# Kernel tuning notes

Measured on AMD Instinct MI355X. Metric: run time of the kernel, lower is better.

## Reference

```python
import jax, jax.numpy as jnp
from jax import lax
import numpy as np

CONF_THRESH = 0.015
NMS_DIST = 4
BORDER = 4
RED = 8


def setup_inputs() -> dict:
    key = jax.random.key(0)
    k1, k2, k3, k4, k5 = jax.random.split(key, 5)
    B, C, H, W = 32, 128, 64, 64
    MID, NCLS = 256, RED * RED + 1
    return {
        "x": jax.random.normal(k1, (B, C, H, W), dtype=jnp.float32),
        "w1": jax.random.normal(k2, (MID, C, 3, 3), dtype=jnp.float32) * 0.05,
        "b1": jax.random.normal(k3, (MID,), dtype=jnp.float32) * 0.05,
        "w2": jax.random.normal(k4, (NCLS, MID, 1, 1), dtype=jnp.float32) * 0.05,
        "b2": jax.random.normal(k5, (NCLS,), dtype=jnp.float32) * 0.05,
    }


def _conv3x3(x, w, b):
    y = lax.conv_general_dilated(
        x, w, window_strides=(1, 1), padding="SAME",
        dimension_numbers=("NCHW", "OIHW", "NCHW"))
    return y + b[None, :, None, None]


def _max_pool(s, r):
    # s: [B, H, W]; infinity-norm neighborhood max, window (2r+1)x(2r+1)
    return lax.reduce_window(
        s, -jnp.inf, lax.max,
        window_dimensions=(1, 2 * r + 1, 2 * r + 1),
        window_strides=(1, 1, 1), padding="SAME")


def _grid_nms(scores, r, iters=8):
    # Iterated local-max suppression; converges to the greedy (sorted-by-score)
    # grid NMS of the original nms_fast routine for distinct scores.
    zeros = jnp.zeros_like(scores)
    max_mask = (scores == _max_pool(scores, r)) & (scores > 0)
    for _ in range(iters):
        supp = _max_pool(max_mask.astype(scores.dtype), r) > 0
        supp_scores = jnp.where(supp, zeros, scores)
        new_max = (supp_scores == _max_pool(supp_scores, r)) & (supp_scores > 0)
        max_mask = max_mask | (new_max & ~supp)
    return jnp.where(max_mask, scores, zeros)


def reference(x, w1, b1, w2, b2):
    B, _, hh, ww = x.shape
    h = jax.nn.relu(_conv3x3(x, w1, b1))                       # [B, mid, hh, ww]
    semi = jnp.einsum("bchw,oc->bohw", h, w2[:, :, 0, 0]) + b2[None, :, None, None]
    dense = jax.nn.softmax(semi, axis=1)                        # [B, 65, hh, ww]
    nodust = dense[:, :-1]                                      # drop dust bin
    # depth-to-space: [B,64,hh,ww] -> [B, hh*8, ww*8]
    heat = nodust.transpose(0, 2, 3, 1).reshape(B, hh, ww, RED, RED)
    heat = heat.transpose(0, 1, 3, 2, 4).reshape(B, hh * RED, ww * RED)
    # confidence threshold
    scores = jnp.where(heat >= CONF_THRESH, heat, 0.0)
    # grid-based NMS (dense keep-map formulation of nms_fast)
    kept = _grid_nms(scores, NMS_DIST)
    # border removal
    Hi, Wi = hh * RED, ww * RED
    yy = jnp.arange(Hi)
    xx = jnp.arange(Wi)
    border = ((yy[:, None] >= BORDER) & (yy[:, None] < Hi - BORDER) &
              (xx[None, :] >= BORDER) & (xx[None, :] < Wi - BORDER))
    return kept * border[None, :, :].astype(kept.dtype)
```

## Files before the change

### kernel.cpp

```cpp
#include <hip/hip_runtime.h>
#include <hip/hip_bf16.h>
#include <stdint.h>

#define BATCH 32
#define CIN 128
#define HH 64
#define WW 64
#define MID 256
#define NCLS 65
#define HI 512
#define NWORDS 8
#define HBS2 264
#define SEMS 68
#define RMS 68

typedef _Float16 half8 __attribute__((ext_vector_type(8)));
typedef _Float16 half4v __attribute__((ext_vector_type(4)));
typedef _Float16 half2v __attribute__((ext_vector_type(2)));
typedef float f32x4 __attribute__((ext_vector_type(4)));

__global__ __launch_bounds__(256) void prep_wf(
    const float* __restrict__ w1, const float* __restrict__ w2,
    _Float16* __restrict__ w1fh, _Float16* __restrict__ w1fl,
    _Float16* __restrict__ w2fh, _Float16* __restrict__ w2fl,
    int* __restrict__ flags)
{
    if (blockIdx.x == 0 && threadIdx.x < 16) flags[threadIdx.x] = 0;
    const int idx = blockIdx.x * 256 + threadIdx.x;
    if (idx < 294912) {
        const int j = idx & 7, lane = (idx >> 3) & 63, mt = (idx >> 9) & 15;
        const int s = (idx >> 13) & 3, kix = idx >> 15;
        const int m = mt * 16 + (lane & 15);
        const int c = s * 32 + (lane >> 4) * 8 + j;
        const int ky = kix / 3, kx = kix - ky * 3;
        const float v = w1[((m * CIN + c) * 3 + ky) * 3 + kx];
        const _Float16 hi = (_Float16)v;
        w1fh[idx] = hi;
        w1fl[idx] = (_Float16)(v - (float)hi);
    } else {
        const int i2 = idx - 294912;
        const int j = i2 & 7, lane = (i2 >> 3) & 63;
        const int ks = (i2 >> 9) & 7, mt = i2 >> 12;
        const int o = mt * 16 + (lane & 15);
        const int k = ks * 32 + (lane >> 4) * 8 + j;
        const float v = (o < NCLS) ? w2[o * MID + k] : 0.f;
        const _Float16 hi = (_Float16)v;
        w2fh[i2] = hi;
        w2fl[i2] = (_Float16)(v - (float)hi);
    }
}

__global__ __launch_bounds__(256, 3) void head_kernel(
    const float* __restrict__ x,
    const _Float16* __restrict__ w1fh, const _Float16* __restrict__ w1fl,
    const _Float16* __restrict__ w2fh, const _Float16* __restrict__ w2fl,
    const float* __restrict__ b1, const float* __restrict__ b2,
    float* __restrict__ out)
{
    const int b  = blockIdx.z;
    const int y0 = blockIdx.y * 8, x0 = blockIdx.x * 8;
    const int tid = threadIdx.x;
    const int lane = tid & 63, w = tid >> 6;
    const int n = lane & 15, q = lane >> 4;

    __shared__ __align__(16) unsigned char SM[51200];
    char* const xhb = (char*)SM;
    _Float16* const hbh = (_Float16*)SM;
    _Float16* const hbl = hbh + 32 * HBS2;
    float* const sem  = (float*)(SM + 33792);
    float* const rinv = sem + 32 * SEMS;

    const float* xb = x + (size_t)b * CIN * HH * WW;
    for (int i = tid; i < 6400; i += 256) {
        const int c2 = i / 100, pos = i - c2 * 100;
        const int r = pos / 10, cc = pos - r * 10;
        const int gy = y0 - 1 + r, gx = x0 - 1 + cc;
        float v0 = 0.f, v1 = 0.f;
        if ((unsigned)gy < HH && (unsigned)gx < WW) {
            const float* p = xb + (c2 * 2 * HH + gy) * WW + gx;
            v0 = p[0]; v1 = p[HH * WW];
        }
        const _Float16 h0 = (_Float16)v0, h1 = (_Float16)v1;
        half2v hi = {h0, h1};
        half2v lo = {(_Float16)(v0 - (float)h0), (_Float16)(v1 - (float)h1)};
        const int slot = (c2 >> 2) ^ (pos & 15);
        char* p16 = xhb + pos * 256 + (slot << 4) + (c2 & 3) * 4;
        *(half2v*)p16 = hi;
        *(half2v*)(p16 + 25600) = lo;
    }
    __syncthreads();

    f32x4 acc[4][4];
#pragma unroll
    for (int i = 0; i < 4; ++i)
#pragma unroll
        for (int t = 0; t < 4; ++t) acc[i][t] = (f32x4){0.f, 0.f, 0.f, 0.f};

    int bposT[4];
#pragma unroll
    for (int t = 0; t < 4; ++t)
        bposT[t] = (t * 2 + (n >> 3)) * 10 + (n & 7);

    for (int kix = 0; kix < 9; ++kix) {
        const int ky = kix / 3;
        const int koff = ky * 10 + (kix - ky * 3);
#pragma unroll
        for (int s = 0; s < 4; ++s) {
            half8 Bh[4], Bl[4];
#pragma unroll
            for (int t = 0; t < 4; ++t) {
                const int pos = bposT[t] + koff;
                const int byteoff = pos * 256 +
                    ((((s << 2) + q) ^ (pos & 15)) << 4);
                Bh[t] = *(const half8*)(xhb + byteoff);
                Bl[t] = *(const half8*)(xhb + 25600 + byteoff);
            }
#pragma unroll
            for (int i = 0; i < 4; ++i) {
                const size_t o = (size_t)(kix * 4 + s) * 8192 +
                                 (w * 4 + i) * 512 + lane * 8;
                const half8 Ah = *(const half8*)(w1fh + o);
                const half8 Al = *(const half8*)(w1fl + o);
#pragma unroll
                for (int t = 0; t < 4; ++t) {
                    acc[i][t] = __builtin_amdgcn_mfma_f32_16x16x32_f16(
                        Ah, Bh[t], acc[i][t], 0, 0, 0);
                    acc[i][t] = __builtin_amdgcn_mfma_f32_16x16x32_f16(
                        Ah, Bl[t], acc[i][t], 0, 0, 0);
                    acc[i][t] = __builtin_amdgcn_mfma_f32_16x16x32_f16(
                        Al, Bh[t], acc[i][t], 0, 0, 0);
                }
            }
        }
    }
    __syncthreads();

    for (int hf = 0; hf < 2; ++hf) {
        if (hf) __syncthreads();
#pragma unroll
        for (int i = 0; i < 4; ++i)
#pragma unroll
            for (int tt = 0; tt < 2; ++tt) {
                const int t = hf * 2 + tt;
                const int p = tt * 16 + n;
                const int m0 = w * 64 + i * 16 + q * 4;
                const f32x4 a = acc[i][t];
                const float4 bv = *(const float4*)(b1 + m0);
                const float h0 = fmaxf(a[0] + bv.x, 0.f);
                const float h1 = fmaxf(a[1] + bv.y, 0.f);
                const float h2 = fmaxf(a[2] + bv.z, 0.f);
                const float h3 = fmaxf(a[3] + bv.w, 0.f);
                half4v hh = {(_Float16)h0, (_Float16)h1,
                             (_Float16)h2, (_Float16)h3};
                half4v hl = {(_Float16)(h0 - (float)hh[0]),
                             (_Float16)(h1 - (float)hh[1]),
                             (_Float16)(h2 - (float)hh[2]),
                             (_Float16)(h3 - (float)hh[3])};
                *(half4v*)(hbh + p * HBS2 + m0) = hh;
                *(half4v*)(hbl + p * HBS2 + m0) = hl;
            }
        __syncthreads();
        {
            const int nt = w & 1;
            const int mt0 = (w < 2) ? 0 : 3;
            const int nmt = (w < 2) ? 3 : 2;
            const int pb = nt * 16 + n;
            f32x4 a2[3];
#pragma unroll
            for (int j = 0; j < 3; ++j) a2[j] = (f32x4){0.f, 0.f, 0.f, 0.f};
#pragma unroll
            for (int ks = 0; ks < 8; ++ks) {
                const int ad = pb * HBS2 + ks * 32 + q * 8;
                const half8 B2h = *(const half8*)(hbh + ad);
                const half8 B2l = *(const half8*)(hbl + ad);
#pragma unroll
                for (int j = 0; j < 3; ++j)
                    if (j < nmt) {
                        const size_t o = (size_t)((mt0 + j) * 8 + ks) * 512 +
                                         lane * 8;
                        const half8 A2h = *(const half8*)(w2fh + o);
                        const half8 A2l = *(const half8*)(w2fl + o);
                        a2[j] = __builtin_amdgcn_mfma_f32_16x16x32_f16(
                            A2h, B2h, a2[j], 0, 0, 0);
                        a2[j] = __builtin_amdgcn_mfma_f32_16x16x32_f16(
                            A2h, B2l, a2[j], 0, 0, 0);
                        a2[j] = __builtin_amdgcn_mfma_f32_16x16x32_f16(
                            A2l, B2h, a2[j], 0, 0, 0);
                    }
            }
#pragma unroll
            for (int j = 0; j < 3; ++j)
                if (j < nmt) {
                    const int o0 = (mt0 + j) * 16 + q * 4;
#pragma unroll
                    for (int r2 = 0; r2 < 4; ++r2) {
                        const int o = o0 + r2;
                        if (o < NCLS)
                            sem[pb * SEMS + o] = a2[j][r2] + b2[o];
                    }
                }
        }
        __syncthreads();
        if (tid < 128) {
            const int p = tid >> 2, q4 = tid & 3;
            const int o0 = q4 * 17;
            const int o1 = (o0 + 17 < NCLS) ? o0 + 17 : NCLS;
            float mx = -1e30f;
            for (int o = o0; o < o1; ++o)
                mx = fmaxf(mx, sem[p * SEMS + o]);
            mx = fmaxf(mx, __shfl_xor(mx, 1));
            mx = fmaxf(mx, __shfl_xor(mx, 2));
            float ssum = 0.f;
            for (int o = o0; o < o1; ++o) {
                float e = __expf(sem[p * SEMS + o] - mx);
                sem[p * SEMS + o] = e;
                ssum += e;
            }
            ssum += __shfl_xor(ssum, 1);
            ssum += __shfl_xor(ssum, 2);
            if (q4 == 0) rinv[p] = 1.f / ssum;
        }
        __syncthreads();
        for (int t2 = tid; t2 < 2048; t2 += 256) {
            const int p = t2 >> 6, o = t2 & 63;
            float v = sem[p * SEMS + o] * rinv[p];
            if (!(v >= 0.015f)) v = 0.f;
            const int P = hf * 32 + p;
            const int py = P >> 3, px = P & 7;
            const int row = (y0 + py) * 8 + (o >> 3);
            const int col = (x0 + px) * 8 + (o & 7);
            out[((size_t)b * HI + row) * HI + col] = v;
        }
    }
}

__device__ __forceinline__ void nms_hmax_phase(
    const float* __restrict__ Sb, const uint64_t* __restrict__ sup,
    float* __restrict__ rm, int ty, int tx, int tid, int rbase)
{
    const int lane = tid & 63;
    for (int k = tid; k < 640; k += 256) {
        const int rr = k >> 4, g = k & 15;
        const int r = rbase + rr;
        const int gy = ty - 4 + r;
        const int x4 = g * 4;
        const uint64_t* sr = sup + r * 3;
        float own[4] = {0.f, 0.f, 0.f, 0.f};
        float halo[4] = {0.f, 0.f, 0.f, 0.f};
        if ((unsigned)gy < HI) {
            const float* row = Sb + (size_t)gy * HI;
            const float4 o4 = *(const float4*)(row + tx + x4);
            own[0] = o4.x; own[1] = o4.y; own[2] = o4.z; own[3] = o4.w;
            const uint64_t w1 = sr[1];
#pragma unroll
            for (int cc = 0; cc < 4; ++cc)
                if ((w1 >> (x4 + cc)) & 1ull) own[cc] = 0.f;
            if (g == 0 && tx >= 4) {
                const float4 h4 = *(const float4*)(row + tx - 4);
                halo[0] = h4.x; halo[1] = h4.y; halo[2] = h4.z; halo[3] = h4.w;
                const uint64_t w0 = sr[0];
#pragma unroll
                for (int cc = 0; cc < 4; ++cc)
                    if ((w0 >> (60 + cc)) & 1ull) halo[cc] = 0.f;
            } else if (g == 15 && tx + 64 < HI) {
                const float4 h4 = *(const float4*)(row + tx + 64);
                halo[0] = h4.x; halo[1] = h4.y; halo[2] = h4.z; halo[3] = h4.w;
                const uint64_t w2 = sr[2];
#pragma unroll
                for (int cc = 0; cc < 4; ++cc)
                    if ((w2 >> cc) & 1ull) halo[cc] = 0.f;
            }
        }
        float v[12];
#pragma unroll
        for (int cc = 0; cc < 4; ++cc) {
            v[4 + cc] = own[cc];
            v[cc]     = __shfl(own[cc], lane - 1);
            v[8 + cc] = __shfl(own[cc], lane + 1);
        }
        if (g == 0) {
#pragma unroll
            for (int cc = 0; cc < 4; ++cc) v[cc] = halo[cc];
        } else if (g == 15) {
#pragma unroll
            for (int cc = 0; cc < 4; ++cc) v[8 + cc] = halo[cc];
        }
        const float m4567 = fmaxf(fmaxf(v[4],v[5]), fmaxf(v[6],v[7]));
        const float m23 = fmaxf(v[2],v[3]), m89 = fmaxf(v[8],v[9]);
        const float o0 = fmaxf(fmaxf(fmaxf(v[0],v[1]), m23),
                               fmaxf(m4567, v[8]));
        const float o1 = fmaxf(fmaxf(v[1], m23), fmaxf(m4567, m89));
        const float o2 = fmaxf(fmaxf(m23, m4567), fmaxf(m89, v[10]));
        const float o3 = fmaxf(fmaxf(v[3], m4567),
                               fmaxf(fmaxf(m89, v[10]), v[11]));
        *(float4*)(rm + rr * RMS + x4) = make_float4(o0,o1,o2,o3);
    }
}

__global__ __launch_bounds__(256, 8) void nms_iter(
    const float* __restrict__ S, const uint64_t* __restrict__ Min,
    uint64_t* __restrict__ Mout, int* __restrict__ flags, int chk, int set)
{
    const int b = blockIdx.z;
    const int bx = blockIdx.x;
    const int ty = blockIdx.y * 64, tx = bx * 64;
    const int tid = threadIdx.x;

    if (chk >= 0 && flags[chk] == 0) {
        for (int y = tid; y < 64; y += 256)
            Mout[((size_t)b * HI + ty + y) * NWORDS + bx] =
                Min[((size_t)b * HI + ty + y) * NWORDS + bx];
        return;
    }

    __shared__ uint64_t smw[80 * 3];
    __shared__ uint64_t hd[80 * 3];
    __shared__ uint64_t sup[72 * 3];
    __shared__ __align__(16) float rm[40 * RMS];

    const float* Sb = S + (size_t)b * HI * HI;
    int chg = 0;

    if (Min) {
        if (tid < 240) {
            const int i = tid / 3, j = tid % 3;
            const int yy = ty - 8 + i;
            const int wj = bx - 1 + j;
            uint64_t v = 0;
            if ((unsigned)yy < HI && (unsigned)wj < NWORDS)
                v = Min[((size_t)b * HI + yy) * NWORDS + wj];
            smw[tid] = v;
        }
        __syncthreads();
        if (tid < 240) {
            const int j = tid % 3;
            const uint64_t c = smw[tid];
            const uint64_t l = j > 0 ? smw[tid - 1] : 0ull;
            const uint64_t r = j < 2 ? smw[tid + 1] : 0ull;
            uint64_t d = c;
#pragma unroll
            for (int s = 1; s <= 4; ++s)
                d |= (c >> s) | (r << (64 - s)) | (c << s) | (l >> (64 - s));
            hd[tid] = d;
        }
        __syncthreads();
        if (tid < 216) {
            uint64_t v = 0;
#pragma unroll
            for (int k = 0; k < 9; ++k) v |= hd[tid + 3 * k];
            sup[tid] = v;
        }
        __syncthreads();
    } else {
        if (tid < 240) smw[tid] = 0;
        if (tid < 216) sup[tid] = 0;
        __syncthreads();
    }

    for (int half = 0; half < 2; ++half) {
        const int rbase = half * 32;
        nms_hmax_phase(Sb, sup, rm, ty, tx, tid, rbase);
        __syncthreads();
        {
            const int wv = tid >> 6, lane = tid & 63;
            const int rb = wv * 8;
            const int ybase = rbase + rb;
            float ring[9];
#pragma unroll
            for (int k = 0; k < 8; ++k) ring[k] = rm[(rb + k) * RMS + lane];
#pragma unroll
            for (int qq = 0; qq < 8; ++qq) {
                const int y = ybase + qq;
                ring[(qq + 8) % 9] = rm[(rb + qq + 8) * RMS + lane];
                float mv = ring[0];
#pragma unroll
                for (int k = 1; k < 9; ++k) mv = fmaxf(mv, ring[k]);
                float c = Sb[(size_t)(ty + y) * HI + tx + lane];
                if ((sup[(y + 4) * 3 + 1] >> lane) & 1ull) c = 0.f;
                const uint64_t oldw = smw[(y + 8) * 3 + 1];
                const bool keep = ((oldw >> lane) & 1ull) ||
                                  (c > 0.f && c == mv);
                const uint64_t word = __ballot(keep);
                if (lane == 0) {
                    Mout[((size_t)b * HI + ty + y) * NWORDS + bx] = word;
                    if (word != oldw) chg = 1;
                }
            }
        }
        __syncthreads();
    }
    if (set >= 0 && (tid & 63) == 0 && chg) flags[set] = 1;
}

__global__ __launch_bounds__(256, 8) void nms_last(
    const float* __restrict__ S, const uint64_t* __restrict__ Min,
    float* __restrict__ out, const int* __restrict__ flags)
{
    const int b = blockIdx.z;
    const int bx = blockIdx.x;
    const int ty = blockIdx.y * 64, tx = bx * 64;
    const int tid = threadIdx.x;

    const float* Sb = S + (size_t)b * HI * HI;

    if (flags[7] == 0) {
        for (int k = tid; k < 1024; k += 256) {
            const int r = k >> 4, c4 = k & 15;
            const int gy = ty + r;
            const int gx0 = tx + c4 * 4;
            const uint64_t w = Min[((size_t)b * HI + gy) * NWORDS + bx];
            float4 v = *(const float4*)(Sb + (size_t)gy * HI + gx0);
            float* pv = (float*)&v;
            const bool rowok = (gy >= 4) && (gy < HI - 4);
#pragma unroll
            for (int cc = 0; cc < 4; ++cc) {
                const int xx = gx0 + cc;
                const bool keep = rowok && (xx >= 4) && (xx < HI - 4) &&
                                  ((w >> ((c4 * 4 + cc) & 63)) & 1ull);
                if (!keep) pv[cc] = 0.f;
            }
            *(float4*)(out + ((size_t)b * HI + gy) * HI + gx0) = v;
        }
        return;
    }

    __shared__ uint64_t smw[80 * 3];
    __shared__ uint64_t hd[80 * 3];
    __shared__ uint64_t sup[72 * 3];
    __shared__ __align__(16) float rm[40 * RMS];

    if (tid < 240) {
        const int i = tid / 3, j = tid % 3;
        const int yy = ty - 8 + i;
        const int wj = bx - 1 + j;
        uint64_t v = 0;
        if ((unsigned)yy < HI && (unsigned)wj < NWORDS)
            v = Min[((size_t)b * HI + yy) * NWORDS + wj];
        smw[tid] = v;
    }
    __syncthreads();
    if (tid < 240) {
        const int j = tid % 3;
        const uint64_t c = smw[tid];
        const uint64_t l = j > 0 ? smw[tid - 1] : 0ull;
        const uint64_t r = j < 2 ? smw[tid + 1] : 0ull;
        uint64_t d = c;
#pragma unroll
        for (int s = 1; s <= 4; ++s)
            d |= (c >> s) | (r << (64 - s)) | (c << s) | (l >> (64 - s));
        hd[tid] = d;
    }
    __syncthreads();
    if (tid < 216) {
        uint64_t v = 0;
#pragma unroll
        for (int k = 0; k < 9; ++k) v |= hd[tid + 3 * k];
        sup[tid] = v;
    }
    __syncthreads();

    for (int half = 0; half < 2; ++half) {
        const int rbase = half * 32;
        nms_hmax_phase(Sb, sup, rm, ty, tx, tid, rbase);
        __syncthreads();
        {
            const int wv = tid >> 6, lane = tid & 63;
            const int rb = wv * 8;
            const int ybase = rbase + rb;
            float ring[9];
#pragma unroll
            for (int k = 0; k < 8; ++k) ring[k] = rm[(rb + k) * RMS + lane];
#pragma unroll
            for (int qq = 0; qq < 8; ++qq) {
                const int y = ybase + qq;
                ring[(qq + 8) % 9] = rm[(rb + qq + 8) * RMS + lane];
                float mv = ring[0];
#pragma unroll
                for (int k = 1; k < 9; ++k) mv = fmaxf(mv, ring[k]);
                const int gy = ty + y, gx = tx + lane;
                const float corig = Sb[(size_t)gy * HI + gx];
                float c = corig;
                if ((sup[(y + 4) * 3 + 1] >> lane) & 1ull) c = 0.f;
                const uint64_t oldw = smw[(y + 8) * 3 + 1];
                const bool keep = ((oldw >> lane) & 1ull) ||
                                  (c > 0.f && c == mv);
                const bool border = (gy >= 4) && (gy < HI - 4) &&
                                    (gx >= 4) && (gx < HI - 4);
                out[((size_t)b * HI + gy) * HI + gx] =
                    (keep && border) ? corig : 0.f;
            }
        }
        __syncthreads();
    }
}

__global__ __launch_bounds__(256) void finalize_bits(
    float* __restrict__ S, const uint64_t* __restrict__ Mw)
{
    const int i4 = blockIdx.x * 256 + threadIdx.x;
    const size_t base = (size_t)i4 * 4;
    const int x = (int)(base & 511);
    const int y = (int)((base >> 9) & 511);
    const int bb = (int)(base >> 18);
    const uint64_t w = Mw[((size_t)bb * HI + y) * NWORDS + (x >> 6)];
    float4 v = ((const float4*)S)[i4];
    float* pv = (float*)&v;
    const bool rowok = (y >= 4) && (y < HI - 4);
#pragma unroll
    for (int cc = 0; cc < 4; ++cc) {
        const int xx = x + cc;
        const bool keep = rowok && (xx >= 4) && (xx < HI - 4) &&
                          ((w >> (xx & 63)) & 1ull);
        if (!keep) pv[cc] = 0.f;
    }
    ((float4*)S)[i4] = v;
}

extern "C" void kernel_launch(void* const* d_in, const int* in_sizes, int n_in,
                              void* d_out, int out_size, void* d_ws, size_t ws_size,
                              hipStream_t stream) {
    const float* x  = (const float*)d_in[0];
    const float* w1 = (const float*)d_in[1];
    const float* b1 = (const float*)d_in[2];
    const float* w2 = (const float*)d_in[3];
    const float* b2 = (const float*)d_in[4];
    float* out = (float*)d_out;

    char* wsb = (char*)d_ws;
    _Float16* w1fh = (_Float16*)(wsb);
    _Float16* w1fl = (_Float16*)(wsb + 0x90000);
    _Float16* w2fh = (_Float16*)(wsb + 0x120000);
    _Float16* w2fl = (_Float16*)(wsb + 0x130000);
    int* flags     = (int*)(wsb + 0x13B000);
    uint64_t* MA   = (uint64_t*)(wsb + 0x140000);
    uint64_t* MB   = (uint64_t*)(wsb + 0x240000);

    const size_t S_OFF = 0x340000;
    const size_t S_BYTES = (size_t)BATCH * HI * HI * 4;
    const bool use_ws = ws_size >= S_OFF + S_BYTES;
    float* S = use_ws ? (float*)(wsb + S_OFF) : out;

    prep_wf<<<1232, 256, 0, stream>>>(w1, w2, w1fh, w1fl, w2fh, w2fl, flags);
    head_kernel<<<dim3(8, 8, BATCH), 256, 0, stream>>>(
        x, w1fh, w1fl, w2fh, w2fl, b1, b2, S);

    dim3 g(NWORDS, 8, BATCH);
    nms_iter<<<g, 256, 0, stream>>>(S, nullptr, MA, flags, -1, -1);
    nms_iter<<<g, 256, 0, stream>>>(S, MA, MB, flags, -1, 1);
    nms_iter<<<g, 256, 0, stream>>>(S, MB, MA, flags, 1, 2);
    nms_iter<<<g, 256, 0, stream>>>(S, MA, MB, flags, 2, 3);
    nms_iter<<<g, 256, 0, stream>>>(S, MB, MA, flags, 3, 4);
    nms_iter<<<g, 256, 0, stream>>>(S, MA, MB, flags, 4, 5);
    nms_iter<<<g, 256, 0, stream>>>(S, MB, MA, flags, 5, 6);
    nms_iter<<<g, 256, 0, stream>>>(S, MA, MB, flags, 6, 7);

    if (use_ws) {
        nms_last<<<g, 256, 0, stream>>>(S, MB, out, flags);
    } else {
        nms_iter<<<g, 256, 0, stream>>>(S, MB, MA, flags, 7, -1);
        const int nf4 = BATCH * HI * HI / 4;
        finalize_bits<<<nf4 / 256, 256, 0, stream>>>(out, MA);
    }
}
```

Baseline: 495.4 us.

## Halve head kernel shared memory by staging input channels in two halves

The head kernel now loads the input tile in two channel halves, running the conv K-loop over each half, so its shared buffer shrinks from 51200 to 25600 bytes. The 1x1 conv and softmax epilogue now works on 16 pixels at a time over four rounds instead of 32 pixels over two. The 65th class row goes to one rotating wave per round. Launch bounds rise from 3 to 4 blocks per CU to exploit the smaller LDS footprint, at the cost of more barriers and register pressure that may cause spills.

```diff
diff --git a/kernel.cpp b/kernel.cpp
--- a/kernel.cpp
+++ b/kernel.cpp
@@ -50,7 +50,7 @@
     }
 }
 
-__global__ __launch_bounds__(256, 3) void head_kernel(
+__global__ __launch_bounds__(256, 4) void head_kernel(
     const float* __restrict__ x,
     const _Float16* __restrict__ w1fh, const _Float16* __restrict__ w1fl,
     const _Float16* __restrict__ w2fh, const _Float16* __restrict__ w2fl,
@@ -63,32 +63,12 @@
     const int lane = tid & 63, w = tid >> 6;
     const int n = lane & 15, q = lane >> 4;
 
-    __shared__ __align__(16) unsigned char SM[51200];
+    __shared__ __align__(16) unsigned char SM[25600];
     char* const xhb = (char*)SM;
     _Float16* const hbh = (_Float16*)SM;
-    _Float16* const hbl = hbh + 32 * HBS2;
-    float* const sem  = (float*)(SM + 33792);
-    float* const rinv = sem + 32 * SEMS;
-
-    const float* xb = x + (size_t)b * CIN * HH * WW;
-    for (int i = tid; i < 6400; i += 256) {
-        const int c2 = i / 100, pos = i - c2 * 100;
-        const int r = pos / 10, cc = pos - r * 10;
-        const int gy = y0 - 1 + r, gx = x0 - 1 + cc;
-        float v0 = 0.f, v1 = 0.f;
-        if ((unsigned)gy < HH && (unsigned)gx < WW) {
-            const float* p = xb + (c2 * 2 * HH + gy) * WW + gx;
-            v0 = p[0]; v1 = p[HH * WW];
-        }
-        const _Float16 h0 = (_Float16)v0, h1 = (_Float16)v1;
-        half2v hi = {h0, h1};
-        half2v lo = {(_Float16)(v0 - (float)h0), (_Float16)(v1 - (float)h1)};
-        const int slot = (c2 >> 2) ^ (pos & 15);
-        char* p16 = xhb + pos * 256 + (slot << 4) + (c2 & 3) * 4;
-        *(half2v*)p16 = hi;
-        *(half2v*)(p16 + 25600) = lo;
-    }
-    __syncthreads();
+    _Float16* const hbl = hbh + 16 * HBS2;
+    float* const sem  = (float*)(SM + 16896);
+    float* const rinv = sem + 16 * SEMS;
 
     f32x4 acc[4][4];
 #pragma unroll
@@ -101,107 +81,132 @@
     for (int t = 0; t < 4; ++t)
         bposT[t] = (t * 2 + (n >> 3)) * 10 + (n & 7);
 
-    for (int kix = 0; kix < 9; ++kix) {
-        const int ky = kix / 3;
-        const int koff = ky * 10 + (kix - ky * 3);
-#pragma unroll
-        for (int s = 0; s < 4; ++s) {
-            half8 Bh[4], Bl[4];
-#pragma unroll
-            for (int t = 0; t < 4; ++t) {
-                const int pos = bposT[t] + koff;
-                const int byteoff = pos * 256 +
-                    ((((s << 2) + q) ^ (pos & 15)) << 4);
-                Bh[t] = *(const half8*)(xhb + byteoff);
-                Bl[t] = *(const half8*)(xhb + 25600 + byteoff);
-            }
-#pragma unroll
-            for (int i = 0; i < 4; ++i) {
-                const size_t o = (size_t)(kix * 4 + s) * 8192 +
-                                 (w * 4 + i) * 512 + lane * 8;
-                const half8 Ah = *(const half8*)(w1fh + o);
-                const half8 Al = *(const half8*)(w1fl + o);
+    const float* xb = x + (size_t)b * CIN * HH * WW;
+
+    for (int half = 0; half < 2; ++half) {
+        if (half) __syncthreads();
+        for (int i = tid; i < 3200; i += 256) {
+            const int c2h = i / 100, pos = i - c2h * 100;
+            const int r = pos / 10, cc = pos - r * 10;
+            const int gy = y0 - 1 + r, gx = x0 - 1 + cc;
+            float v0 = 0.f, v1 = 0.f;
+            if ((unsigned)gy < HH && (unsigned)gx < WW) {
+                const float* p =
+                    xb + (((half * 32 + c2h) * 2) * HH + gy) * WW + gx;
+                v0 = p[0]; v1 = p[HH * WW];
+            }
+            const _Float16 h0 = (_Float16)v0, h1 = (_Float16)v1;
+            half2v hi = {h0, h1};
+            half2v lo = {(_Float16)(v0 - (float)h0),
+                         (_Float16)(v1 - (float)h1)};
+            const int slot = (c2h >> 2) ^ (pos & 7);
+            char* p16 = xhb + pos * 128 + (slot << 4) + (c2h & 3) * 4;
+            *(half2v*)p16 = hi;
+            *(half2v*)(p16 + 12800) = lo;
+        }
+        __syncthreads();
+
+        for (int kix = 0; kix < 9; ++kix) {
+            const int ky = kix / 3;
+            const int koff = ky * 10 + (kix - ky * 3);
+#pragma unroll
+            for (int sl = 0; sl < 2; ++sl) {
+                half8 Bh[4], Bl[4];
 #pragma unroll
                 for (int t = 0; t < 4; ++t) {
-                    acc[i][t] = __builtin_amdgcn_mfma_f32_16x16x32_f16(
-                        Ah, Bh[t], acc[i][t], 0, 0, 0);
-                    acc[i][t] = __builtin_amdgcn_mfma_f32_16x16x32_f16(
-                        Ah, Bl[t], acc[i][t], 0, 0, 0);
-                    acc[i][t] = __builtin_amdgcn_mfma_f32_16x16x32_f16(
-                        Al, Bh[t], acc[i][t], 0, 0, 0);
+                    const int pos = bposT[t] + koff;
+                    const int byteoff = pos * 128 +
+                        ((((sl << 2) + q) ^ (pos & 7)) << 4);
+                    Bh[t] = *(const half8*)(xhb + byteoff);
+                    Bl[t] = *(const half8*)(xhb + 12800 + byteoff);
                 }
+                const int s = half * 2 + sl;
+#pragma unroll
+                for (int i = 0; i < 4; ++i) {
+                    const size_t o = (size_t)(kix * 4 + s) * 8192 +
+                                     (w * 4 + i) * 512 + lane * 8;
+                    const half8 Ah = *(const half8*)(w1fh + o);
+                    const half8 Al = *(const half8*)(w1fl + o);
+#pragma unroll
+                    for (int t = 0; t < 4; ++t) {
+                        acc[i][t] = __builtin_amdgcn_mfma_f32_16x16x32_f16(
+                            Ah, Bh[t], acc[i][t], 0, 0, 0);
+                        acc[i][t] = __builtin_amdgcn_mfma_f32_16x16x32_f16(
+                            Ah, Bl[t], acc[i][t], 0, 0, 0);
+                        acc[i][t] = __builtin_amdgcn_mfma_f32_16x16x32_f16(
+                            Al, Bh[t], acc[i][t], 0, 0, 0);
+                    }
+                }
             }
         }
     }
     __syncthreads();
 
-    for (int hf = 0; hf < 2; ++hf) {
-        if (hf) __syncthreads();
-#pragma unroll
-        for (int i = 0; i < 4; ++i)
-#pragma unroll
-            for (int tt = 0; tt < 2; ++tt) {
-                const int t = hf * 2 + tt;
-                const int p = tt * 16 + n;
-                const int m0 = w * 64 + i * 16 + q * 4;
-                const f32x4 a = acc[i][t];
-                const float4 bv = *(const float4*)(b1 + m0);
-                const float h0 = fmaxf(a[0] + bv.x, 0.f);
-                const float h1 = fmaxf(a[1] + bv.y, 0.f);
-                const float h2 = fmaxf(a[2] + bv.z, 0.f);
-                const float h3 = fmaxf(a[3] + bv.w, 0.f);
-                half4v hh = {(_Float16)h0, (_Float16)h1,
-                             (_Float16)h2, (_Float16)h3};
-                half4v hl = {(_Float16)(h0 - (float)hh[0]),
-                             (_Float16)(h1 - (float)hh[1]),
-                             (_Float16)(h2 - (float)hh[2]),
-                             (_Float16)(h3 - (float)hh[3])};
-                *(half4v*)(hbh + p * HBS2 + m0) = hh;
-                *(half4v*)(hbl + p * HBS2 + m0) = hl;
-            }
+#pragma unroll
+    for (int qt = 0; qt < 4; ++qt) {
+        if (qt) __syncthreads();
+#pragma unroll
+        for (int i = 0; i < 4; ++i) {
+            const int m0 = w * 64 + i * 16 + q * 4;
+            const f32x4 a = acc[i][qt];
+            const float4 bv = *(const float4*)(b1 + m0);
+            const float h0 = fmaxf(a[0] + bv.x, 0.f);
+            const float h1 = fmaxf(a[1] + bv.y, 0.f);
+            const float h2 = fmaxf(a[2] + bv.z, 0.f);
+            const float h3 = fmaxf(a[3] + bv.w, 0.f);
+            half4v hh = {(_Float16)h0, (_Float16)h1,
+                         (_Float16)h2, (_Float16)h3};
+            half4v hl = {(_Float16)(h0 - (float)hh[0]),
+                         (_Float16)(h1 - (float)hh[1]),
+                         (_Float16)(h2 - (float)hh[2]),
+                         (_Float16)(h3 - (float)hh[3])};
+            *(half4v*)(hbh + n * HBS2 + m0) = hh;
+            *(half4v*)(hbl + n * HBS2 + m0) = hl;
+        }
         __syncthreads();
         {
-            const int nt = w & 1;
-            const int mt0 = (w < 2) ? 0 : 3;
-            const int nmt = (w < 2) ? 3 : 2;
-            const int pb = nt * 16 + n;
-            f32x4 a2[3];
-#pragma unroll
-            for (int j = 0; j < 3; ++j) a2[j] = (f32x4){0.f, 0.f, 0.f, 0.f};
+            const int extra = qt & 3;
+            f32x4 a2[2];
+            a2[0] = (f32x4){0.f, 0.f, 0.f, 0.f};
+            a2[1] = (f32x4){0.f, 0.f, 0.f, 0.f};
 #pragma unroll
             for (int ks = 0; ks < 8; ++ks) {
-                const int ad = pb * HBS2 + ks * 32 + q * 8;
+                const int ad = n * HBS2 + ks * 32 + q * 8;
                 const half8 B2h = *(const half8*)(hbh + ad);
                 const half8 B2l = *(const half8*)(hbl + ad);
-#pragma unroll
-                for (int j = 0; j < 3; ++j)
-                    if (j < nmt) {
-                        const size_t o = (size_t)((mt0 + j) * 8 + ks) * 512 +
-                                         lane * 8;
-                        const half8 A2h = *(const half8*)(w2fh + o);
-                        const half8 A2l = *(const half8*)(w2fl + o);
-                        a2[j] = __builtin_amdgcn_mfma_f32_16x16x32_f16(
-                            A2h, B2h, a2[j], 0, 0, 0);
-                        a2[j] = __builtin_amdgcn_mfma_f32_16x16x32_f16(
-                            A2h, B2l, a2[j], 0, 0, 0);
-                        a2[j] = __builtin_amdgcn_mfma_f32_16x16x32_f16(
-                            A2l, B2h, a2[j], 0, 0, 0);
-                    }
-            }
-#pragma unroll
-            for (int j = 0; j < 3; ++j)
-                if (j < nmt) {
-                    const int o0 = (mt0 + j) * 16 + q * 4;
-#pragma unroll
-                    for (int r2 = 0; r2 < 4; ++r2) {
-                        const int o = o0 + r2;
-                        if (o < NCLS)
-                            sem[pb * SEMS + o] = a2[j][r2] + b2[o];
-                    }
+                {
+                    const size_t o = (size_t)(w * 8 + ks) * 512 + lane * 8;
+                    const half8 A2h = *(const half8*)(w2fh + o);
+                    const half8 A2l = *(const half8*)(w2fl + o);
+                    a2[0] = __builtin_amdgcn_mfma_f32_16x16x32_f16(
+                        A2h, B2h, a2[0], 0, 0, 0);
+                    a2[0] = __builtin_amdgcn_mfma_f32_16x16x32_f16(
+                        A2h, B2l, a2[0], 0, 0, 0);
+                    a2[0] = __builtin_amdgcn_mfma_f32_16x16x32_f16(
+                        A2l, B2h, a2[0], 0, 0, 0);
                 }
-        }
-        __syncthreads();
-        if (tid < 128) {
+                if (w == extra) {
+                    const size_t o = (size_t)(4 * 8 + ks) * 512 + lane * 8;
+                    const half8 A2h = *(const half8*)(w2fh + o);
+                    const half8 A2l = *(const half8*)(w2fl + o);
+                    a2[1] = __builtin_amdgcn_mfma_f32_16x16x32_f16(
+                        A2h, B2h, a2[1], 0, 0, 0);
+                    a2[1] = __builtin_amdgcn_mfma_f32_16x16x32_f16(
+                        A2h, B2l, a2[1], 0, 0, 0);
+                    a2[1] = __builtin_amdgcn_mfma_f32_16x16x32_f16(
+                        A2l, B2h, a2[1], 0, 0, 0);
+                }
+            }
+#pragma unroll
+            for (int r2 = 0; r2 < 4; ++r2) {
+                const int o = w * 16 + q * 4 + r2;
+                sem[n * SEMS + o] = a2[0][r2] + b2[o];
+            }
+            if (w == extra && q == 0)
+                sem[n * SEMS + 64] = a2[1][0] + b2[64];
+        }
+        __syncthreads();
+        if (tid < 64) {
             const int p = tid >> 2, q4 = tid & 3;
             const int o0 = q4 * 17;
             const int o1 = (o0 + 17 < NCLS) ? o0 + 17 : NCLS;
@@ -221,11 +226,11 @@
             if (q4 == 0) rinv[p] = 1.f / ssum;
         }
         __syncthreads();
-        for (int t2 = tid; t2 < 2048; t2 += 256) {
+        for (int t2 = tid; t2 < 1024; t2 += 256) {
             const int p = t2 >> 6, o = t2 & 63;
             float v = sem[p * SEMS + o] * rinv[p];
             if (!(v >= 0.015f)) v = 0.f;
-            const int P = hf * 32 + p;
+            const int P = qt * 16 + p;
             const int py = P >> 3, px = P & 7;
             const int row = (y0 + py) * 8 + (o >> 3);
             const int col = (x0 + px) * 8 + (o & 7);
```

Result: slower. 590.7 us (+19.2%).
